# Optimization experiments

Hardware: AMD Instinct MI355X
Metric: run time of the kernel (lower is better)

The kernel has to match this reference:

```python
import jax, jax.numpy as jnp
import numpy as np

B, S, L = 128, 512, 20  # batch, max seq length, g.max_word_length
VOCAB = 10000


def setup_inputs() -> dict:
    key = jax.random.key(0)
    k1, k2, k3 = jax.random.split(key, 3)
    lost_unit_id_seqs = jax.random.randint(k1, (B, S), 0, VOCAB, dtype=jnp.int32)
    # lengths in [L, S] so every batch element has viable spans
    lost_lengths = jax.random.randint(k2, (B,), L, S + 1, dtype=jnp.int32)
    p_weights = jax.random.uniform(k3, (B, S, L), dtype=jnp.float32)
    return {
        "lost_unit_id_seqs": lost_unit_id_seqs,
        "lost_lengths": lost_lengths,
        "p_weights": p_weights,
        "max_word_length": L,
    }


def reference(lost_unit_id_seqs, lost_lengths, p_weights, max_word_length):
    b, s = lost_unit_id_seqs.shape
    l = max_word_length
    n = b * s * l  # static upper bound on number of viable spans

    # _propose_candidates: enumerate all (start, span_length) pairs
    starts = jnp.arange(s, dtype=jnp.int32)[None, :, None]          # [1,S,1]
    lens = jnp.arange(1, l + 1, dtype=jnp.int32)[None, None, :]      # [1,1,L]
    ends = starts + lens - 1                                          # [1,S,L]

    viable = ends < lost_lengths[:, None, None]                       # [B,S,L] bool
    shape = viable.shape
    start_candidates = jnp.broadcast_to(starts, shape)
    end_candidates = jnp.broadcast_to(ends, shape)
    len_candidates = jnp.broadcast_to(lens, shape)
    batch_indices = jnp.broadcast_to(
        jnp.arange(b, dtype=jnp.int32)[:, None, None], shape)

    # boolean-mask stream compaction with static size (viable entries first,
    # tail padded with index 0; true count = viable.sum())
    flat_viable = viable.reshape(-1)
    idx = jnp.nonzero(flat_viable, size=n, fill_value=0)[0]           # [N]

    viable_starts = start_candidates.reshape(-1)[idx]
    viable_ends = end_candidates.reshape(-1)[idx]
    viable_lengths = len_candidates.reshape(-1)[idx]
    viable_batch_indices = batch_indices.reshape(-1)[idx]
    viable_p_weights = p_weights.reshape(-1)[idx]

    # 2D advanced-index gather of unit ids for each viable span
    max_length = jnp.max(lost_lengths)
    word_pos = jnp.minimum(
        viable_starts[:, None] + jnp.arange(l, dtype=jnp.int32)[None, :],
        max_length - 1)                                               # [N,L]
    viable_unit_id_seqs = lost_unit_id_seqs[viable_batch_indices[:, None], word_pos]

    return (viable, viable_batch_indices, viable_starts, viable_ends,
            viable_lengths, viable_unit_id_seqs, viable_p_weights,
            start_candidates, end_candidates, len_candidates)
```

## Files before the change

kernel.cpp:

```cpp
#include <hip/hip_runtime.h>
#include <stdint.h>

#define TPB 256
#define BB  128
#define SS  512
#define LLW 20
#define NN  (BB * SS * LLW)
#define KPT 4
#define KPB (TPB * KPT)
#define MAXROWS 8
#define RSTRIDE 516

static __device__ __forceinline__ void preamble(const int* __restrict__ lens,
                                                int* shC, int* shM, int* shLen,
                                                int t) {
  int len0 = (t < BB) ? lens[t] : 0;
  shLen[t] = len0;
  shC[t] = (t < BB) ? (LLW * len0 - (LLW * (LLW - 1)) / 2) : 0;
  shM[t] = len0;
  for (int off = 1; off < TPB; off <<= 1) {
    __syncthreads();
    int aC = shC[t]; int bC = (t >= off) ? shC[t - off] : 0;
    int aM = shM[t]; int bM = shM[t ^ off];
    __syncthreads();
    shC[t] = aC + bC;
    shM[t] = (aM > bM) ? aM : bM;
  }
  __syncthreads();
}

static __device__ __forceinline__ int batch_of(int k, const int* shC) {
  int lo = 0, hi = BB - 1;
  while (lo < hi) {
    int mid = (lo + hi) >> 1;
    if (shC[mid] > k) hi = mid; else lo = mid + 1;
  }
  return lo;
}

static __device__ __forceinline__ void invert(int k, const int* shC,
                                              const int* shLen, int K,
                                              int* pb, int* ps, int* pj) {
  int b = 0, s = 0, j = 0;
  if (k < K) {
    b = batch_of(k, shC);
    int base = (b == 0) ? 0 : shC[b - 1];
    int m    = k - base;
    int lenb = shLen[b];
    int full = LLW * (lenb - LLW + 1);
    if (m < full) {
      s = m / LLW;
      j = m - s * LLW;
    } else {
      int Cb = shC[b] - base;
      int tt = Cb - m;
      float rf = (sqrtf(8.0f * (float)tt + 1.0f) - 1.0f) * 0.5f;
      int r = (int)(rf + 0.5f);
      if (r * (r + 1) / 2 < tt) r++;
      if (r > 1 && r * (r - 1) / 2 >= tt) r--;
      s = lenb - r;
      j = r * (r + 1) / 2 - tt;
    }
  }
  *pb = b; *ps = s; *pj = j;
}

__global__ __launch_bounds__(TPB) void span_full(
    const int* __restrict__ seqs,
    const int* __restrict__ lens,
    const float* __restrict__ pw,
    float* __restrict__ out) {
  __shared__ int shC[TPB], shM[TPB], shLen[TPB];
  __shared__ int sBS[KPB];
  __shared__ int sRows[MAXROWS * RSTRIDE];
  const int t = threadIdx.x;
  preamble(lens, shC, shM, shLen, t);
  const int K  = shC[BB - 1];
  const int ml = shM[0];

  const int gid    = blockIdx.x * TPB + t;
  const int k0     = gid * KPT;
  const int blk_k0 = blockIdx.x * KPB;
  const size_t Nz  = (size_t)NN;

  int kq0 = blk_k0;           if (kq0 > K - 1) kq0 = K - 1;
  int kq1 = blk_k0 + KPB - 1; if (kq1 > K - 1) kq1 = K - 1;
  const int bf = batch_of(kq0, shC);
  int nrows = (blk_k0 < K) ? (batch_of(kq1, shC) - bf + 1) : 0;
  if (nrows > MAXROWS) nrows = MAXROWS;
  {
    const int4* src = (const int4*)(seqs + (size_t)bf * SS);
    for (int q = t; q < nrows * (SS / 4); q += TPB) {
      int lin = q << 2;
      int r = lin >> 9, p = lin & (SS - 1);
      *(int4*)(sRows + r * RSTRIDE + p) = src[q];
    }
  }

  {
    float qv[KPT], qsc[KPT], qec[KPT], qlc[KPT];
#pragma unroll
    for (int i = 0; i < KPT; i++) {
      int f   = k0 + i;
      int row = f / LLW;
      int jj  = f - row * LLW;
      int b2  = row >> 9;
      int s2  = row & (SS - 1);
      int e2  = s2 + jj;
      qv[i]  = (e2 < shLen[b2]) ? 1.0f : 0.0f;
      qsc[i] = (float)s2; qec[i] = (float)e2; qlc[i] = (float)(jj + 1);
    }
    *(float4*)(out + k0)           = make_float4(qv[0], qv[1], qv[2], qv[3]);
    *(float4*)(out + 26 * Nz + k0) = make_float4(qsc[0], qsc[1], qsc[2], qsc[3]);
    *(float4*)(out + 27 * Nz + k0) = make_float4(qec[0], qec[1], qec[2], qec[3]);
    *(float4*)(out + 28 * Nz + k0) = make_float4(qlc[0], qlc[1], qlc[2], qlc[3]);
  }
  {
    int b, s, j;
    invert(k0, shC, shLen, K, &b, &s, &j);
    float qb[KPT], qs[KPT], qe[KPT], ql[KPT], qp[KPT];
#pragma unroll
    for (int i = 0; i < KPT; i++) {
      int ki = k0 + i;
      int vb = 0, vs = 0, vj = 0;
      if (ki < K) {
        vb = b; vs = s; vj = j;
        j++;
        int lenb = shLen[b];
        int cs = lenb - s; if (cs > LLW) cs = LLW;
        if (j >= cs) { j = 0; s++; if (s >= lenb) { s = 0; b++; } }
      }
      qb[i] = (float)vb; qs[i] = (float)vs;
      qe[i] = (float)(vs + vj); ql[i] = (float)(vj + 1);
      qp[i] = pw[((size_t)vb * SS + vs) * LLW + vj];
      sBS[t * KPT + i] = (vb << 16) | vs;
    }
    *(float4*)(out + Nz + k0)      = make_float4(qb[0], qb[1], qb[2], qb[3]);
    *(float4*)(out + 2 * Nz + k0)  = make_float4(qs[0], qs[1], qs[2], qs[3]);
    *(float4*)(out + 3 * Nz + k0)  = make_float4(qe[0], qe[1], qe[2], qe[3]);
    *(float4*)(out + 4 * Nz + k0)  = make_float4(ql[0], ql[1], ql[2], ql[3]);
    *(float4*)(out + 25 * Nz + k0) = make_float4(qp[0], qp[1], qp[2], qp[3]);
  }
  __syncthreads();
  {
    int ml1 = ml - 1;
    float4* udst = (float4*)(out + 5 * Nz + (size_t)blk_k0 * LLW);
    for (int c = 0; c < (KPB * (LLW / 4)) / TPB; c++) {
      int chunk = t + c * TPB;
      int krow  = chunk / 5;
      int e0    = (chunk - krow * 5) << 2;
      int bs    = sBS[krow];
      int b = bs >> 16, s = bs & 0xFFFF;
      int p0 = s + e0;     if (p0 > ml1) p0 = ml1;
      int p1 = s + e0 + 1; if (p1 > ml1) p1 = ml1;
      int p2 = s + e0 + 2; if (p2 > ml1) p2 = ml1;
      int p3 = s + e0 + 3; if (p3 > ml1) p3 = ml1;
      float4 v;
      int ridx = b - bf;
      if ((unsigned)ridx < (unsigned)nrows) {
        const int* rp = sRows + ridx * RSTRIDE;
        v.x = (float)rp[p0]; v.y = (float)rp[p1];
        v.z = (float)rp[p2]; v.w = (float)rp[p3];
      } else {
        const int* rp = seqs + (size_t)b * SS;
        v.x = (float)rp[p0]; v.y = (float)rp[p1];
        v.z = (float)rp[p2]; v.w = (float)rp[p3];
      }
      udst[chunk] = v;
    }
  }
}

extern "C" void kernel_launch(void* const* d_in, const int* in_sizes, int n_in,
                              void* d_out, int out_size, void* d_ws, size_t ws_size,
                              hipStream_t stream) {
  const int*   seqs = (const int*)d_in[0];
  const int*   lens = (const int*)d_in[1];
  const float* pw   = (const float*)d_in[2];
  float* out = (float*)d_out;

  span_full<<<NN / KPB, TPB, 0, stream>>>(seqs, lens, pw, out);
}
```

Measured before the change: 161.8 us.

## Split prefix-scan into separate pre-kernel and simplify main span kernel

Moves the per-block batch-length prefix scan and max reduction into a tiny single-block pre-kernel that writes results to workspace, so each main block only loads the precomputed tables instead of running a 256-wide scan with many barriers. It drops the shared-memory staging of sequence rows in favour of direct global (cached) reads, halves items per thread to double the block count, and adds a min-blocks launch bound to raise occupancy. It adds a second kernel launch plus a dependency, and smaller per-thread stores (float2 instead of float4).

```diff
diff --git a/kernel.cpp b/kernel.cpp
--- a/kernel.cpp
+++ b/kernel.cpp
@@ -6,27 +6,29 @@
 #define SS  512
 #define LLW 20
 #define NN  (BB * SS * LLW)
-#define KPT 4
+#define KPT 2
 #define KPB (TPB * KPT)
-#define MAXROWS 8
-#define RSTRIDE 516
+#define NBLK (NN / KPB)
 
-static __device__ __forceinline__ void preamble(const int* __restrict__ lens,
-                                                int* shC, int* shM, int* shLen,
-                                                int t) {
-  int len0 = (t < BB) ? lens[t] : 0;
-  shLen[t] = len0;
-  shC[t] = (t < BB) ? (LLW * len0 - (LLW * (LLW - 1)) / 2) : 0;
-  shM[t] = len0;
-  for (int off = 1; off < TPB; off <<= 1) {
+__global__ __launch_bounds__(BB) void span_pre(const int* __restrict__ lens,
+                                               int* __restrict__ ws) {
+  __shared__ int sC[BB], sM[BB];
+  const int t = threadIdx.x;
+  const int len = lens[t];
+  sC[t] = LLW * len - (LLW * (LLW - 1)) / 2;
+  sM[t] = len;
+  for (int off = 1; off < BB; off <<= 1) {
     __syncthreads();
-    int aC = shC[t]; int bC = (t >= off) ? shC[t - off] : 0;
-    int aM = shM[t]; int bM = shM[t ^ off];
+    int aC = sC[t]; int bC = (t >= off) ? sC[t - off] : 0;
+    int aM = sM[t]; int bM = sM[t ^ off];
     __syncthreads();
-    shC[t] = aC + bC;
-    shM[t] = (aM > bM) ? aM : bM;
+    sC[t] = aC + bC;
+    sM[t] = (aM > bM) ? aM : bM;
   }
   __syncthreads();
+  ws[t]      = sC[t];
+  ws[BB + t] = len;
+  if (t == 0) ws[2 * BB] = sM[0];
 }
 
 static __device__ __forceinline__ int batch_of(int k, const int* shC) {
@@ -65,56 +67,24 @@
   *pb = b; *ps = s; *pj = j;
 }
 
-__global__ __launch_bounds__(TPB) void span_full(
+__global__ __launch_bounds__(TPB, 4) void span_main(
     const int* __restrict__ seqs,
-    const int* __restrict__ lens,
     const float* __restrict__ pw,
+    const int* __restrict__ ws,
     float* __restrict__ out) {
-  __shared__ int shC[TPB], shM[TPB], shLen[TPB];
+  __shared__ int shC[BB], shLen[BB];
   __shared__ int sBS[KPB];
-  __shared__ int sRows[MAXROWS * RSTRIDE];
   const int t = threadIdx.x;
-  preamble(lens, shC, shM, shLen, t);
-  const int K  = shC[BB - 1];
-  const int ml = shM[0];
+  if (t < BB) { shC[t] = ws[t]; shLen[t] = ws[BB + t]; }
+  const int K  = ws[BB - 1];
+  const int ml = ws[2 * BB];
+  __syncthreads();
 
   const int gid    = blockIdx.x * TPB + t;
   const int k0     = gid * KPT;
   const int blk_k0 = blockIdx.x * KPB;
   const size_t Nz  = (size_t)NN;
 
-  int kq0 = blk_k0;           if (kq0 > K - 1) kq0 = K - 1;
-  int kq1 = blk_k0 + KPB - 1; if (kq1 > K - 1) kq1 = K - 1;
-  const int bf = batch_of(kq0, shC);
-  int nrows = (blk_k0 < K) ? (batch_of(kq1, shC) - bf + 1) : 0;
-  if (nrows > MAXROWS) nrows = MAXROWS;
-  {
-    const int4* src = (const int4*)(seqs + (size_t)bf * SS);
-    for (int q = t; q < nrows * (SS / 4); q += TPB) {
-      int lin = q << 2;
-      int r = lin >> 9, p = lin & (SS - 1);
-      *(int4*)(sRows + r * RSTRIDE + p) = src[q];
-    }
-  }
-
-  {
-    float qv[KPT], qsc[KPT], qec[KPT], qlc[KPT];
-#pragma unroll
-    for (int i = 0; i < KPT; i++) {
-      int f   = k0 + i;
-      int row = f / LLW;
-      int jj  = f - row * LLW;
-      int b2  = row >> 9;
-      int s2  = row & (SS - 1);
-      int e2  = s2 + jj;
-      qv[i]  = (e2 < shLen[b2]) ? 1.0f : 0.0f;
-      qsc[i] = (float)s2; qec[i] = (float)e2; qlc[i] = (float)(jj + 1);
-    }
-    *(float4*)(out + k0)           = make_float4(qv[0], qv[1], qv[2], qv[3]);
-    *(float4*)(out + 26 * Nz + k0) = make_float4(qsc[0], qsc[1], qsc[2], qsc[3]);
-    *(float4*)(out + 27 * Nz + k0) = make_float4(qec[0], qec[1], qec[2], qec[3]);
-    *(float4*)(out + 28 * Nz + k0) = make_float4(qlc[0], qlc[1], qlc[2], qlc[3]);
-  }
   {
     int b, s, j;
     invert(k0, shC, shLen, K, &b, &s, &j);
@@ -135,15 +105,35 @@
       qp[i] = pw[((size_t)vb * SS + vs) * LLW + vj];
       sBS[t * KPT + i] = (vb << 16) | vs;
     }
-    *(float4*)(out + Nz + k0)      = make_float4(qb[0], qb[1], qb[2], qb[3]);
-    *(float4*)(out + 2 * Nz + k0)  = make_float4(qs[0], qs[1], qs[2], qs[3]);
-    *(float4*)(out + 3 * Nz + k0)  = make_float4(qe[0], qe[1], qe[2], qe[3]);
-    *(float4*)(out + 4 * Nz + k0)  = make_float4(ql[0], ql[1], ql[2], ql[3]);
-    *(float4*)(out + 25 * Nz + k0) = make_float4(qp[0], qp[1], qp[2], qp[3]);
+    *(float2*)(out + Nz + k0)      = make_float2(qb[0], qb[1]);
+    *(float2*)(out + 2 * Nz + k0)  = make_float2(qs[0], qs[1]);
+    *(float2*)(out + 3 * Nz + k0)  = make_float2(qe[0], qe[1]);
+    *(float2*)(out + 4 * Nz + k0)  = make_float2(ql[0], ql[1]);
+    *(float2*)(out + 25 * Nz + k0) = make_float2(qp[0], qp[1]);
   }
   __syncthreads();
+
   {
-    int ml1 = ml - 1;
+    float qv[KPT], qsc[KPT], qec[KPT], qlc[KPT];
+#pragma unroll
+    for (int i = 0; i < KPT; i++) {
+      int f   = k0 + i;
+      int row = f / LLW;
+      int jj  = f - row * LLW;
+      int b2  = row >> 9;
+      int s2  = row & (SS - 1);
+      int e2  = s2 + jj;
+      qv[i]  = (e2 < shLen[b2]) ? 1.0f : 0.0f;
+      qsc[i] = (float)s2; qec[i] = (float)e2; qlc[i] = (float)(jj + 1);
+    }
+    *(float2*)(out + k0)           = make_float2(qv[0], qv[1]);
+    *(float2*)(out + 26 * Nz + k0) = make_float2(qsc[0], qsc[1]);
+    *(float2*)(out + 27 * Nz + k0) = make_float2(qec[0], qec[1]);
+    *(float2*)(out + 28 * Nz + k0) = make_float2(qlc[0], qlc[1]);
+  }
+
+  {
+    const int ml1 = ml - 1;
     float4* udst = (float4*)(out + 5 * Nz + (size_t)blk_k0 * LLW);
     for (int c = 0; c < (KPB * (LLW / 4)) / TPB; c++) {
       int chunk = t + c * TPB;
@@ -151,21 +141,14 @@
       int e0    = (chunk - krow * 5) << 2;
       int bs    = sBS[krow];
       int b = bs >> 16, s = bs & 0xFFFF;
+      const int* rp = seqs + (size_t)b * SS;
       int p0 = s + e0;     if (p0 > ml1) p0 = ml1;
       int p1 = s + e0 + 1; if (p1 > ml1) p1 = ml1;
       int p2 = s + e0 + 2; if (p2 > ml1) p2 = ml1;
       int p3 = s + e0 + 3; if (p3 > ml1) p3 = ml1;
       float4 v;
-      int ridx = b - bf;
-      if ((unsigned)ridx < (unsigned)nrows) {
-        const int* rp = sRows + ridx * RSTRIDE;
-        v.x = (float)rp[p0]; v.y = (float)rp[p1];
-        v.z = (float)rp[p2]; v.w = (float)rp[p3];
-      } else {
-        const int* rp = seqs + (size_t)b * SS;
-        v.x = (float)rp[p0]; v.y = (float)rp[p1];
-        v.z = (float)rp[p2]; v.w = (float)rp[p3];
-      }
+      v.x = (float)rp[p0]; v.y = (float)rp[p1];
+      v.z = (float)rp[p2]; v.w = (float)rp[p3];
       udst[chunk] = v;
     }
   }
@@ -178,6 +161,8 @@
   const int*   lens = (const int*)d_in[1];
   const float* pw   = (const float*)d_in[2];
   float* out = (float*)d_out;
+  int*   ws  = (int*)d_ws;
 
-  span_full<<<NN / KPB, TPB, 0, stream>>>(seqs, lens, pw, out);
+  span_pre<<<1, BB, 0, stream>>>(lens, ws);
+  span_main<<<NBLK, TPB, 0, stream>>>(seqs, pw, (const int*)ws, out);
 }
```

Result: no change. 164.9 us (+1.9%).

## Pre-clamp and pre-convert staged rows in LDS and remap block order across XCDs

Applied to the files above, without the earlier changes.

Staged sequence rows now go into shared memory already converted to float and pre-clamped to max_length-1, with padding past the row end. The gather loop can then read four contiguous floats with no per-element clamp or int-to-float conversion. Block indices are also permuted with an interleave of 8 so that consecutive logical blocks land on different dies (MI355X has 8 XCDs), spreading work and possibly improving L2 locality. The trade-off is that staging is now a scalar per-element load instead of vectorized int4 copies, and it uses a larger shared-memory footprint.

```diff
diff --git a/kernel.cpp b/kernel.cpp
--- a/kernel.cpp
+++ b/kernel.cpp
@@ -8,8 +8,10 @@
 #define NN  (BB * SS * LLW)
 #define KPT 4
 #define KPB (TPB * KPT)
+#define NBLK (NN / KPB)
 #define MAXROWS 8
-#define RSTRIDE 516
+#define RS  536
+#define RW  532
 
 static __device__ __forceinline__ void preamble(const int* __restrict__ lens,
                                                 int* shC, int* shM, int* shLen,
@@ -70,17 +72,20 @@
     const int* __restrict__ lens,
     const float* __restrict__ pw,
     float* __restrict__ out) {
-  __shared__ int shC[TPB], shM[TPB], shLen[TPB];
-  __shared__ int sBS[KPB];
-  __shared__ int sRows[MAXROWS * RSTRIDE];
+  __shared__ int   shC[TPB], shM[TPB], shLen[TPB];
+  __shared__ int   sBS[KPB];
+  __shared__ float sRowF[MAXROWS * RS];
   const int t = threadIdx.x;
   preamble(lens, shC, shM, shLen, t);
-  const int K  = shC[BB - 1];
-  const int ml = shM[0];
+  const int K   = shC[BB - 1];
+  const int ml1 = shM[0] - 1;
 
-  const int gid    = blockIdx.x * TPB + t;
+  const int bid  = (int)blockIdx.x;
+  const int vbid = (bid & 7) * (NBLK / 8) + (bid >> 3);
+
+  const int gid    = vbid * TPB + t;
   const int k0     = gid * KPT;
-  const int blk_k0 = blockIdx.x * KPB;
+  const int blk_k0 = vbid * KPB;
   const size_t Nz  = (size_t)NN;
 
   int kq0 = blk_k0;           if (kq0 > K - 1) kq0 = K - 1;
@@ -88,12 +93,11 @@
   const int bf = batch_of(kq0, shC);
   int nrows = (blk_k0 < K) ? (batch_of(kq1, shC) - bf + 1) : 0;
   if (nrows > MAXROWS) nrows = MAXROWS;
-  {
-    const int4* src = (const int4*)(seqs + (size_t)bf * SS);
-    for (int q = t; q < nrows * (SS / 4); q += TPB) {
-      int lin = q << 2;
-      int r = lin >> 9, p = lin & (SS - 1);
-      *(int4*)(sRows + r * RSTRIDE + p) = src[q];
+  for (int r = 0; r < nrows; r++) {
+    const int* rp = seqs + (size_t)(bf + r) * SS;
+    for (int p = t; p < RW; p += TPB) {
+      int pp = (p > ml1) ? ml1 : p;
+      sRowF[r * RS + p] = (float)rp[pp];
     }
   }
 
@@ -142,8 +146,8 @@
     *(float4*)(out + 25 * Nz + k0) = make_float4(qp[0], qp[1], qp[2], qp[3]);
   }
   __syncthreads();
+
   {
-    int ml1 = ml - 1;
     float4* udst = (float4*)(out + 5 * Nz + (size_t)blk_k0 * LLW);
     for (int c = 0; c < (KPB * (LLW / 4)) / TPB; c++) {
       int chunk = t + c * TPB;
@@ -151,18 +155,17 @@
       int e0    = (chunk - krow * 5) << 2;
       int bs    = sBS[krow];
       int b = bs >> 16, s = bs & 0xFFFF;
-      int p0 = s + e0;     if (p0 > ml1) p0 = ml1;
-      int p1 = s + e0 + 1; if (p1 > ml1) p1 = ml1;
-      int p2 = s + e0 + 2; if (p2 > ml1) p2 = ml1;
-      int p3 = s + e0 + 3; if (p3 > ml1) p3 = ml1;
+      int ridx = b - bf;
       float4 v;
-      int ridx = b - bf;
       if ((unsigned)ridx < (unsigned)nrows) {
-        const int* rp = sRows + ridx * RSTRIDE;
-        v.x = (float)rp[p0]; v.y = (float)rp[p1];
-        v.z = (float)rp[p2]; v.w = (float)rp[p3];
+        const float* fp = sRowF + ridx * RS + s + e0;
+        v.x = fp[0]; v.y = fp[1]; v.z = fp[2]; v.w = fp[3];
       } else {
         const int* rp = seqs + (size_t)b * SS;
+        int p0 = s + e0;     if (p0 > ml1) p0 = ml1;
+        int p1 = s + e0 + 1; if (p1 > ml1) p1 = ml1;
+        int p2 = s + e0 + 2; if (p2 > ml1) p2 = ml1;
+        int p3 = s + e0 + 3; if (p3 > ml1) p3 = ml1;
         v.x = (float)rp[p0]; v.y = (float)rp[p1];
         v.z = (float)rp[p2]; v.w = (float)rp[p3];
       }
@@ -179,5 +182,5 @@
   const float* pw   = (const float*)d_in[2];
   float* out = (float*)d_out;
 
-  span_full<<<NN / KPB, TPB, 0, stream>>>(seqs, lens, pw, out);
+  span_full<<<NBLK, TPB, 0, stream>>>(seqs, lens, pw, out);
 }
```

New measurement: 166.0 us. +2.6%, slower.
